# Kernel optimization log

Measured on AMD Instinct MI355X. Metric: run time of the kernel, lower is better.

Reference implementation:

```python
import math
import jax, jax.numpy as jnp
import numpy as np

EMBED = 512
HEADS = 2
HEAD_DIM = EMBED // HEADS


def setup_inputs() -> dict:
    key = jax.random.key(0)
    ks = jax.random.split(key, 10)
    s = 1.0 / math.sqrt(EMBED)
    return {
        "text_embeds": jax.random.normal(ks[0], (64, 32, EMBED), jnp.float32),
        "video_embeds": jax.random.normal(ks[1], (128, 64, EMBED), jnp.float32),
        "Wq": jax.random.normal(ks[2], (EMBED, EMBED), jnp.float32) * s,
        "bq": jnp.zeros((EMBED,), jnp.float32),
        "Wk": jax.random.normal(ks[3], (EMBED, EMBED), jnp.float32) * s,
        "bk": jnp.zeros((EMBED,), jnp.float32),
        "Wv": jax.random.normal(ks[4], (EMBED, EMBED), jnp.float32) * s,
        "bv": jnp.zeros((EMBED,), jnp.float32),
        "Wo": jax.random.normal(ks[5], (EMBED, EMBED), jnp.float32) * s,
        "bo": jnp.zeros((EMBED,), jnp.float32),
    }


def reference(text_embeds, video_embeds, Wq, bq, Wk, bk, Wv, bv, Wo, bo):
    num_texts, num_words, _ = text_embeds.shape
    num_vids, num_frames, _ = video_embeds.shape
    # projections (torch Linear: x @ W.T + b)
    q = (text_embeds @ Wq.T + bq).reshape(num_texts, num_words, HEADS, HEAD_DIM)
    k = (video_embeds @ Wk.T + bk).reshape(num_vids, num_frames, HEADS, HEAD_DIM)
    v = (video_embeds @ Wv.T + bv).reshape(num_vids, num_frames, HEADS, HEAD_DIM)
    # 5D cross attention logits: [vids, texts, heads, frames, words]
    logits = jnp.einsum('avhd,bthd->abhvt', k, q) / math.sqrt(HEAD_DIM)
    weights = jax.nn.softmax(logits, axis=3)  # softmax over frames
    attn = jnp.einsum('avhd,abhvt->abhtd', v, weights)  # [a,b,h,t,d]
    # faithful to torch: reshape (a,b,h,t,d) -> (a,b,t,h*d) in row-major order
    attn = attn.reshape(num_vids, num_texts, num_words, EMBED)
    attn = attn.mean(axis=0)  # [texts, words, embed]
    return attn @ Wo.T + bo
```

## Files before the change

### kernel.cpp

```cpp
#include <hip/hip_runtime.h>
#include <hip/hip_bf16.h>
#include <math.h>

#define EMBED  512
#define HEADS  2
#define HDIM   256
#define NTEXT  64
#define NWORD  32
#define NVID   128
#define NFRM   64

typedef __attribute__((ext_vector_type(8))) short      short8;
typedef __attribute__((ext_vector_type(8))) unsigned short ushort8;
typedef __attribute__((ext_vector_type(4))) float      float4v;
typedef __attribute__((ext_vector_type(4))) unsigned short ushort4v;

__device__ __forceinline__ unsigned short f2bf(float x) {
    __hip_bfloat16 h = __float2bfloat16(x);
    return *(unsigned short*)&h;
}
__device__ __forceinline__ float bf2f(unsigned short u) {
    __hip_bfloat16 h = *(__hip_bfloat16*)&u;
    return __bfloat162float(h);
}

__device__ __forceinline__ void gload_lds16(unsigned short* dst, const unsigned short* src) {
#if __has_builtin(__builtin_amdgcn_global_load_lds)
    __builtin_amdgcn_global_load_lds((const __attribute__((address_space(1))) void*)src,
                                     (__attribute__((address_space(3))) void*)dst,
                                     16, 0, 0);
#else
    *(ushort8*)dst = *(const ushort8*)src;
#endif
}

__global__ __launch_bounds__(256)
void cvt5(const float* __restrict__ s0, const float* __restrict__ s1,
          const float* __restrict__ s2, const float* __restrict__ s3,
          const float* __restrict__ s4, unsigned short* __restrict__ dst) {
    const int y = blockIdx.y;
    const float* s; size_t off; int n4;
    if (y == 0)      { s = s0; off = 0;       n4 = 262144;  }
    else if (y == 1) { s = s1; off = 1048576; n4 = 1048576; }
    else if (y == 2) { s = s2; off = 5242880; n4 = 65536;   }
    else if (y == 3) { s = s3; off = 5505024; n4 = 65536;   }
    else             { s = s4; off = 5767168; n4 = 65536;   }
    unsigned short* d = dst + off;
    for (int i = blockIdx.x * 256 + threadIdx.x; i < n4; i += 512 * 256) {
        float4v f = ((const float4v*)s)[i];
        ((ushort4v*)d)[i] = (ushort4v){f2bf(f.x), f2bf(f.y), f2bf(f.z), f2bf(f.w)};
    }
}

__global__ __launch_bounds__(256)
void proj_qkv(const unsigned short* __restrict__ text, const unsigned short* __restrict__ video,
              const unsigned short* __restrict__ Wqb, const float* __restrict__ bq,
              const unsigned short* __restrict__ Wkb, const float* __restrict__ bk,
              const unsigned short* __restrict__ Wvb, const float* __restrict__ bv,
              unsigned short* __restrict__ qout,
              unsigned short* __restrict__ Kgf, unsigned short* __restrict__ Vgf) {
    const int mb = blockIdx.x, nb = blockIdx.y;
    const int bj = nb * 64;
    const unsigned short *A, *W;
    const float* bias;
    int op, arow, a = 0;
    if (mb < 32)       { op = 0; A = text;  W = Wqb; bias = bq; arow = mb * 64; }
    else if (mb < 160) { op = 1; A = video; W = Wkb; bias = bk; a = mb - 32;  arow = a * 64; }
    else               { op = 2; A = video; W = Wvb; bias = bv; a = mb - 160; arow = a * 64; }

    __shared__ __align__(16) unsigned char smem[32768];
    unsigned short (*Eb)[72] = (unsigned short (*)[72])smem;

    const int tid = threadIdx.x;
    const int w = tid >> 6, lane = tid & 63;
    const int lm = lane & 15, qd = lane >> 4;

    float4v acc[4];
    #pragma unroll
    for (int nt = 0; nt < 4; ++nt) acc[nt] = (float4v){0.f, 0.f, 0.f, 0.f};

    auto STAGE = [&](int buf, int k0) {
        unsigned short* AbL = (unsigned short*)(smem + buf * 16384);
        unsigned short* WbL = (unsigned short*)(smem + buf * 16384 + 8192);
        #pragma unroll
        for (int it = 0; it < 2; ++it) {
            const int s = tid + it * 256;
            const int r = s >> 3, c8 = s & 7;
            const int sc = (c8 ^ (r & 7)) * 8;
            gload_lds16(&AbL[(size_t)s * 8], &A[(size_t)(arow + r) * 512 + k0 + sc]);
            gload_lds16(&WbL[(size_t)s * 8], &W[(size_t)(bj   + r) * 512 + k0 + sc]);
        }
    };

    STAGE(0, 0);
    __syncthreads();
    int cur = 0;
    for (int ks = 0; ks < 8; ++ks) {
        if (ks < 7) STAGE(cur ^ 1, (ks + 1) * 64);
        const unsigned short* AbL = (const unsigned short*)(smem + cur * 16384);
        const unsigned short* WbL = (const unsigned short*)(smem + cur * 16384 + 8192);
        #pragma unroll
        for (int kq = 0; kq < 2; ++kq) {
            const int scol = (kq * 32 + qd * 8) ^ ((lm & 7) * 8);
            const short8 af = *(const short8*)&AbL[(w * 16 + lm) * 64 + scol];
            #pragma unroll
            for (int nt = 0; nt < 4; ++nt) {
                const short8 bf = *(const short8*)&WbL[(nt * 16 + lm) * 64 + scol];
                acc[nt] = __builtin_amdgcn_mfma_f32_16x16x32_bf16(af, bf, acc[nt], 0, 0, 0);
            }
        }
        __syncthreads();
        cur ^= 1;
    }

    if (op == 0) {
        #pragma unroll
        for (int nt = 0; nt < 4; ++nt) {
            const int c = bj + nt * 16 + lm;
            const float bb = bias[c];
            #pragma unroll
            for (int reg = 0; reg < 4; ++reg) {
                const int r = arow + w * 16 + qd * 4 + reg;
                qout[(size_t)r * 512 + c] = f2bf((acc[nt][reg] + bb) * 0.0625f);
            }
        }
        return;
    }

    const int h = bj >> 8;
    const int bj_rel = bj & 255;

    if (op == 1) {
        #pragma unroll
        for (int nt = 0; nt < 4; ++nt) {
            const int dl = nt * 16 + lm;
            const float bb = bias[bj + dl];
            #pragma unroll
            for (int reg = 0; reg < 4; ++reg)
                Eb[w * 16 + qd * 4 + reg][dl] = f2bf(acc[nt][reg] + bb);
        }
        __syncthreads();
        const size_t base = ((size_t)(h * 128 + a)) * 16384;
        #pragma unroll
        for (int i = 0; i < 2; ++i) {
            const int s = tid + i * 256;
            const int ntf = s >> 7, kqr = (s >> 6) & 1, l = s & 63;
            const int v = ntf * 16 + (l & 15);
            const int dl = kqr * 32 + (l >> 4) * 8;
            ushort8 val = *(const ushort8*)&Eb[v][dl];
            *(ushort8*)&Kgf[base + ((size_t)(ntf * 8 + (bj_rel >> 5) + kqr) * 64 + l) * 8] = val;
        }
    } else {
        #pragma unroll
        for (int nt = 0; nt < 4; ++nt) {
            const int dl = nt * 16 + lm;
            const float bb = bias[bj + dl];
            #pragma unroll
            for (int reg = 0; reg < 4; ++reg)
                Eb[dl][w * 16 + qd * 4 + reg] = f2bf(acc[nt][reg] + bb);
        }
        __syncthreads();
        const size_t base = ((size_t)(h * 128 + a)) * 16384;
        #pragma unroll
        for (int i = 0; i < 2; ++i) {
            const int s = tid + i * 256;
            const int ntr = s >> 7, kqv = (s >> 6) & 1, l = s & 63;
            const int dl = ntr * 16 + (l & 15);
            const int v0 = kqv * 32 + (l >> 4) * 8;
            ushort8 val = *(const ushort8*)&Eb[dl][v0];
            *(ushort8*)&Vgf[base + ((size_t)(((bj_rel >> 4) + ntr) * 2 + kqv) * 64 + l) * 8] = val;
        }
    }
}

__global__ __launch_bounds__(512, 2)
void attn9(const unsigned short* __restrict__ Kgf,
           const unsigned short* __restrict__ Vgf,
           const unsigned short* __restrict__ q,
           unsigned short* __restrict__ partg) {
    const int c  = blockIdx.x;
    const int h  = blockIdx.y;
    const int tg = blockIdx.z;
    const int tid = threadIdx.x;
    const int w = tid >> 6, lane = tid & 63;
    const int lm = lane & 15, qd = lane >> 4;
    const int wt = w >> 1;
    const int fh = w & 1;
    const int b = tg * 4 + wt;

    __shared__ __align__(16) unsigned short Kb[2][16384];
    __shared__ __align__(16) unsigned short Vb[2][16384];
    __shared__ __align__(16) unsigned short Pf[4][2][2][512];
    __shared__ __align__(16) float Ex[4][2][2][16][2];

    short8 qf[2][8];
    #pragma unroll
    for (int mt = 0; mt < 2; ++mt)
        #pragma unroll
        for (int kq = 0; kq < 8; ++kq)
            qf[mt][kq] = *(const short8*)
                &q[((size_t)(b * 32 + mt * 16 + lm)) * 512 + h * 256 + kq * 32 + qd * 8];

    float4v pacc[2][8];
    #pragma unroll
    for (int mt = 0; mt < 2; ++mt)
        #pragma unroll
        for (int nd = 0; nd < 8; ++nd) pacc[mt][nd] = (float4v){0.f, 0.f, 0.f, 0.f};

    const size_t vb0 = (size_t)(h * 128 + c * 16) * 16384;

    #pragma unroll
    for (int i = 0; i < 4; ++i) {
        const int s = tid + i * 512;
        gload_lds16(&Kb[0][(size_t)s * 8], &Kgf[vb0 + (size_t)s * 8]);
        gload_lds16(&Vb[0][(size_t)s * 8], &Vgf[vb0 + (size_t)s * 8]);
    }
    #pragma unroll
    for (int i = 0; i < 4; ++i) {
        const int s = tid + i * 512;
        gload_lds16(&Kb[1][(size_t)s * 8], &Kgf[vb0 + 16384 + (size_t)s * 8]);
        gload_lds16(&Vb[1][(size_t)s * 8], &Vgf[vb0 + 16384 + (size_t)s * 8]);
    }
    __syncthreads();

    for (int ai = 0; ai < 16; ++ai) {
        const int cur = ai & 1;

        float4v lacc[2][2];
        #pragma unroll
        for (int nt = 0; nt < 2; ++nt)
            #pragma unroll
            for (int mt = 0; mt < 2; ++mt) lacc[nt][mt] = (float4v){0.f, 0.f, 0.f, 0.f};
        #pragma unroll
        for (int kq = 0; kq < 8; ++kq) {
            #pragma unroll
            for (int nt = 0; nt < 2; ++nt) {
                const short8 kf = *(const short8*)
                    &Kb[cur][(((fh * 2 + nt) * 8 + kq) * 64 + lane) * 8];
                lacc[nt][0] = __builtin_amdgcn_mfma_f32_16x16x32_bf16(kf, qf[0][kq], lacc[nt][0], 0, 0, 0);
                lacc[nt][1] = __builtin_amdgcn_mfma_f32_16x16x32_bf16(kf, qf[1][kq], lacc[nt][1], 0, 0, 0);
            }
        }

        float m2[2], sv[2], e[2][2][4];
        #pragma unroll
        for (int mt = 0; mt < 2; ++mt) {
            float mm = lacc[0][mt][0];
            #pragma unroll
            for (int nt = 0; nt < 2; ++nt)
                #pragma unroll
                for (int r = 0; r < 4; ++r) mm = fmaxf(mm, lacc[nt][mt][r]);
            mm = fmaxf(mm, __shfl_xor(mm, 16));
            mm = fmaxf(mm, __shfl_xor(mm, 32));
            float ss = 0.f;
            #pragma unroll
            for (int nt = 0; nt < 2; ++nt)
                #pragma unroll
                for (int r = 0; r < 4; ++r) {
                    const float ev = __expf(lacc[nt][mt][r] - mm);
                    e[mt][nt][r] = ev;
                    ss += ev;
                }
            ss += __shfl_xor(ss, 16);
            ss += __shfl_xor(ss, 32);
            m2[mt] = mm; sv[mt] = ss;
            if (qd == 0) {
                Ex[wt][fh][mt][lm][0] = mm;
                Ex[wt][fh][mt][lm][1] = ss;
            }
        }
        __syncthreads();

        #pragma unroll
        for (int mt = 0; mt < 2; ++mt) {
            const float om = Ex[wt][fh ^ 1][mt][lm][0];
            const float os = Ex[wt][fh ^ 1][mt][lm][1];
            const float M   = fmaxf(m2[mt], om);
            const float den = sv[mt] * __expf(m2[mt] - M) + os * __expf(om - M);
            const float fac = __expf(m2[mt] - M) / den;
            #pragma unroll
            for (int nt = 0; nt < 2; ++nt) {
                ushort4v pv;
                pv.x = f2bf(e[mt][nt][0] * fac);
                pv.y = f2bf(e[mt][nt][1] * fac);
                pv.z = f2bf(e[mt][nt][2] * fac);
                pv.w = f2bf(e[mt][nt][3] * fac);
                *(ushort4v*)&Pf[wt][mt][fh][(lm + 16 * (nt * 2 + (qd >> 1))) * 8 + (qd & 1) * 4] = pv;
            }
        }
        __syncthreads();

        #pragma unroll
        for (int kqv = 0; kqv < 2; ++kqv) {
            const short8 pf0 = *(const short8*)&Pf[wt][0][kqv][lane * 8];
            const short8 pf1 = *(const short8*)&Pf[wt][1][kqv][lane * 8];
            #pragma unroll
            for (int nd = 0; nd < 8; ++nd) {
                const short8 vf = *(const short8*)
                    &Vb[cur][(((fh * 8 + nd) * 2 + kqv) * 64 + lane) * 8];
                pacc[0][nd] = __builtin_amdgcn_mfma_f32_16x16x32_bf16(pf0, vf, pacc[0][nd], 0, 0, 0);
                pacc[1][nd] = __builtin_amdgcn_mfma_f32_16x16x32_bf16(pf1, vf, pacc[1][nd], 0, 0, 0);
            }
        }
        __syncthreads();

        if (ai < 14) {
            const size_t kb = vb0 + (size_t)(ai + 2) * 16384;
            #pragma unroll
            for (int i = 0; i < 4; ++i) {
                const int s = tid + i * 512;
                gload_lds16(&Kb[cur][(size_t)s * 8], &Kgf[kb + (size_t)s * 8]);
                gload_lds16(&Vb[cur][(size_t)s * 8], &Vgf[kb + (size_t)s * 8]);
            }
        }
    }

    unsigned short* part = partg + (size_t)c * 1048576;
    #pragma unroll
    for (int mt = 0; mt < 2; ++mt)
        #pragma unroll
        for (int nd = 0; nd < 8; ++nd)
            #pragma unroll
            for (int r = 0; r < 4; ++r) {
                const int t = mt * 16 + qd * 4 + r;
                const int d = fh * 128 + nd * 16 + lm;
                const int row = b * 32 + h * 16 + (t >> 1);
                const int col = (t & 1) * 256 + d;
                part[(size_t)row * 512 + col] = f2bf(pacc[mt][nd][r]);
            }
}

__global__ __launch_bounds__(256)
void reduce8(unsigned short* __restrict__ partg) {
    const size_t i = ((size_t)blockIdx.x * 256 + threadIdx.x) * 8;
    float s[8];
    #pragma unroll
    for (int j = 0; j < 8; ++j) s[j] = 0.f;
    #pragma unroll
    for (int p = 0; p < 8; ++p) {
        ushort8 u = *(const ushort8*)&partg[(size_t)p * 1048576 + i];
        #pragma unroll
        for (int j = 0; j < 8; ++j) s[j] += bf2f(u[j]);
    }
    ushort8 o;
    #pragma unroll
    for (int j = 0; j < 8; ++j) o[j] = f2bf(s[j] * 0.0078125f);
    *(ushort8*)&partg[i] = o;
}

__global__ __launch_bounds__(256)
void proj_o(const unsigned short* __restrict__ Abf, const float* __restrict__ W,
            const float* __restrict__ bias, float* __restrict__ C) {
    __shared__ __align__(16) unsigned short Ab[64][72];
    __shared__ __align__(16) unsigned short Wb[64][72];
    const int tid = threadIdx.x;
    const int bi = blockIdx.x * 64, bj = blockIdx.y * 64;
    const int w = tid >> 6, lane = tid & 63;
    const int lm = lane & 15, qd = lane >> 4;

    float4v acc[4];
    #pragma unroll
    for (int nt = 0; nt < 4; ++nt) acc[nt] = (float4v){0.f, 0.f, 0.f, 0.f};

    for (int k0 = 0; k0 < 512; k0 += 64) {
        #pragma unroll
        for (int it = 0; it < 2; ++it) {
            const int s = tid + it * 256;
            const int r = s >> 3, c8 = (s & 7) * 8;
            *(ushort8*)&Ab[r][c8] = *(const ushort8*)&Abf[(size_t)(bi + r) * 512 + k0 + c8];
        }
        #pragma unroll
        for (int it = 0; it < 4; ++it) {
            const int s = tid + it * 256;
            const int r = s >> 4, c4 = (s & 15) * 4;
            float4v fw = *(const float4v*)&W[(size_t)(bj + r) * 512 + k0 + c4];
            *(ushort4v*)&Wb[r][c4] = (ushort4v){f2bf(fw.x), f2bf(fw.y), f2bf(fw.z), f2bf(fw.w)};
        }
        __syncthreads();
        #pragma unroll
        for (int kq = 0; kq < 2; ++kq) {
            const short8 af = *(const short8*)&Ab[w * 16 + lm][kq * 32 + qd * 8];
            #pragma unroll
            for (int nt = 0; nt < 4; ++nt) {
                const short8 bf = *(const short8*)&Wb[nt * 16 + lm][kq * 32 + qd * 8];
                acc[nt] = __builtin_amdgcn_mfma_f32_16x16x32_bf16(af, bf, acc[nt], 0, 0, 0);
            }
        }
        __syncthreads();
    }
    #pragma unroll
    for (int nt = 0; nt < 4; ++nt) {
        const int cc = bj + nt * 16 + lm;
        const float bb = bias[cc];
        #pragma unroll
        for (int reg = 0; reg < 4; ++reg) {
            const int r = bi + w * 16 + qd * 4 + reg;
            C[(size_t)r * 512 + cc] = acc[nt][reg] + bb;
        }
    }
}

extern "C" void kernel_launch(void* const* d_in, const int* in_sizes, int n_in,
                              void* d_out, int out_size, void* d_ws, size_t ws_size,
                              hipStream_t stream) {
    const float* text  = (const float*)d_in[0];
    const float* video = (const float*)d_in[1];
    const float* Wq = (const float*)d_in[2];
    const float* bq = (const float*)d_in[3];
    const float* Wk = (const float*)d_in[4];
    const float* bk = (const float*)d_in[5];
    const float* Wv = (const float*)d_in[6];
    const float* bv = (const float*)d_in[7];
    const float* Wo = (const float*)d_in[8];
    const float* bo = (const float*)d_in[9];

    unsigned short* Kgf   = (unsigned short*)d_ws;
    unsigned short* Vgf   = (unsigned short*)((char*)d_ws + (8u << 20));
    unsigned short* partg = (unsigned short*)((char*)d_ws + (16u << 20));
    unsigned short* textbf  = partg;
    unsigned short* videobf = partg + 1048576;
    unsigned short* wqbf    = partg + 5242880;
    unsigned short* wkbf    = partg + 5505024;
    unsigned short* wvbf    = partg + 5767168;
    unsigned short* qbf   = (unsigned short*)d_out;
    float*          out   = (float*)d_out;

    cvt5<<<dim3(512, 5), 256, 0, stream>>>(text, video, Wq, Wk, Wv, partg);
    proj_qkv<<<dim3(288, 8), 256, 0, stream>>>(textbf, videobf, wqbf, bq, wkbf, bk,
                                               wvbf, bv, qbf, Kgf, Vgf);
    attn9<<<dim3(8, 2, 16), 512, 0, stream>>>(Kgf, Vgf, qbf, partg);
    reduce8<<<dim3(512), 256, 0, stream>>>(partg);
    proj_o<<<dim3(32, 8), 256, 0, stream>>>(partg, Wo, bo, out);
}
```

Baseline: 166.6 us.

## Enlarge QKV projection tiles to 128x128 with 2x2 warp tiling

```diff
diff --git a/kernel.cpp b/kernel.cpp
--- a/kernel.cpp
+++ b/kernel.cpp
@@ -60,35 +60,37 @@
               unsigned short* __restrict__ qout,
               unsigned short* __restrict__ Kgf, unsigned short* __restrict__ Vgf) {
     const int mb = blockIdx.x, nb = blockIdx.y;
-    const int bj = nb * 64;
+    const int bj = nb * 128;
     const unsigned short *A, *W;
     const float* bias;
-    int op, arow, a = 0;
-    if (mb < 32)       { op = 0; A = text;  W = Wqb; bias = bq; arow = mb * 64; }
-    else if (mb < 160) { op = 1; A = video; W = Wkb; bias = bk; a = mb - 32;  arow = a * 64; }
-    else               { op = 2; A = video; W = Wvb; bias = bv; a = mb - 160; arow = a * 64; }
-
-    __shared__ __align__(16) unsigned char smem[32768];
-    unsigned short (*Eb)[72] = (unsigned short (*)[72])smem;
+    int op, arow0, abase = 0;
+    if (mb < 16)      { op = 0; A = text;  W = Wqb; bias = bq; arow0 = mb * 128; }
+    else if (mb < 80) { op = 1; A = video; W = Wkb; bias = bk; abase = (mb - 16) * 2; arow0 = abase * 64; }
+    else              { op = 2; A = video; W = Wvb; bias = bv; abase = (mb - 80) * 2; arow0 = abase * 64; }
+
+    __shared__ __align__(16) unsigned char smem[65536];
 
     const int tid = threadIdx.x;
     const int w = tid >> 6, lane = tid & 63;
     const int lm = lane & 15, qd = lane >> 4;
-
-    float4v acc[4];
-    #pragma unroll
-    for (int nt = 0; nt < 4; ++nt) acc[nt] = (float4v){0.f, 0.f, 0.f, 0.f};
+    const int wr = w >> 1, wc = w & 1;
+
+    float4v acc[4][4];
+    #pragma unroll
+    for (int rt = 0; rt < 4; ++rt)
+        #pragma unroll
+        for (int ct = 0; ct < 4; ++ct) acc[rt][ct] = (float4v){0.f, 0.f, 0.f, 0.f};
 
     auto STAGE = [&](int buf, int k0) {
-        unsigned short* AbL = (unsigned short*)(smem + buf * 16384);
-        unsigned short* WbL = (unsigned short*)(smem + buf * 16384 + 8192);
-        #pragma unroll
-        for (int it = 0; it < 2; ++it) {
+        unsigned short* AbL = (unsigned short*)(smem + buf * 32768);
+        unsigned short* WbL = (unsigned short*)(smem + buf * 32768 + 16384);
+        #pragma unroll
+        for (int it = 0; it < 4; ++it) {
             const int s = tid + it * 256;
             const int r = s >> 3, c8 = s & 7;
             const int sc = (c8 ^ (r & 7)) * 8;
-            gload_lds16(&AbL[(size_t)s * 8], &A[(size_t)(arow + r) * 512 + k0 + sc]);
-            gload_lds16(&WbL[(size_t)s * 8], &W[(size_t)(bj   + r) * 512 + k0 + sc]);
+            gload_lds16(&AbL[(size_t)s * 8], &A[(size_t)(arow0 + r) * 512 + k0 + sc]);
+            gload_lds16(&WbL[(size_t)s * 8], &W[(size_t)(bj    + r) * 512 + k0 + sc]);
         }
     };
 
@@ -97,17 +99,23 @@
     int cur = 0;
     for (int ks = 0; ks < 8; ++ks) {
         if (ks < 7) STAGE(cur ^ 1, (ks + 1) * 64);
-        const unsigned short* AbL = (const unsigned short*)(smem + cur * 16384);
-        const unsigned short* WbL = (const unsigned short*)(smem + cur * 16384 + 8192);
+        const unsigned short* AbL = (const unsigned short*)(smem + cur * 32768);
+        const unsigned short* WbL = (const unsigned short*)(smem + cur * 32768 + 16384);
         #pragma unroll
         for (int kq = 0; kq < 2; ++kq) {
             const int scol = (kq * 32 + qd * 8) ^ ((lm & 7) * 8);
-            const short8 af = *(const short8*)&AbL[(w * 16 + lm) * 64 + scol];
-            #pragma unroll
-            for (int nt = 0; nt < 4; ++nt) {
-                const short8 bf = *(const short8*)&WbL[(nt * 16 + lm) * 64 + scol];
-                acc[nt] = __builtin_amdgcn_mfma_f32_16x16x32_bf16(af, bf, acc[nt], 0, 0, 0);
-            }
+            short8 af[4], bf[4];
+            #pragma unroll
+            for (int rt = 0; rt < 4; ++rt)
+                af[rt] = *(const short8*)&AbL[(wr * 64 + rt * 16 + lm) * 64 + scol];
+            #pragma unroll
+            for (int ct = 0; ct < 4; ++ct)
+                bf[ct] = *(const short8*)&WbL[(wc * 64 + ct * 16 + lm) * 64 + scol];
+            #pragma unroll
+            for (int rt = 0; rt < 4; ++rt)
+                #pragma unroll
+                for (int ct = 0; ct < 4; ++ct)
+                    acc[rt][ct] = __builtin_amdgcn_mfma_f32_16x16x32_bf16(af[rt], bf[ct], acc[rt][ct], 0, 0, 0);
         }
         __syncthreads();
         cur ^= 1;
@@ -115,35 +123,42 @@
 
     if (op == 0) {
         #pragma unroll
-        for (int nt = 0; nt < 4; ++nt) {
-            const int c = bj + nt * 16 + lm;
-            const float bb = bias[c];
-            #pragma unroll
-            for (int reg = 0; reg < 4; ++reg) {
-                const int r = arow + w * 16 + qd * 4 + reg;
-                qout[(size_t)r * 512 + c] = f2bf((acc[nt][reg] + bb) * 0.0625f);
-            }
-        }
+        for (int rt = 0; rt < 4; ++rt)
+            #pragma unroll
+            for (int ct = 0; ct < 4; ++ct) {
+                const int c = bj + wc * 64 + ct * 16 + lm;
+                const float bb = bias[c];
+                #pragma unroll
+                for (int reg = 0; reg < 4; ++reg) {
+                    const int r = arow0 + wr * 64 + rt * 16 + qd * 4 + reg;
+                    qout[(size_t)r * 512 + c] = f2bf((acc[rt][ct][reg] + bb) * 0.0625f);
+                }
+            }
         return;
     }
 
-    const int h = bj >> 8;
-    const int bj_rel = bj & 255;
+    const int a   = abase + wr;
+    const int bjs = bj + wc * 64;
+    const int h      = bjs >> 8;
+    const int bj_rel = bjs & 255;
+    unsigned short (*Eb)[72] = (unsigned short (*)[72])(smem + w * 9216);
+    const size_t base = ((size_t)(h * 128 + a)) * 16384;
 
     if (op == 1) {
         #pragma unroll
-        for (int nt = 0; nt < 4; ++nt) {
-            const int dl = nt * 16 + lm;
-            const float bb = bias[bj + dl];
-            #pragma unroll
-            for (int reg = 0; reg < 4; ++reg)
-                Eb[w * 16 + qd * 4 + reg][dl] = f2bf(acc[nt][reg] + bb);
-        }
-        __syncthreads();
-        const size_t base = ((size_t)(h * 128 + a)) * 16384;
-        #pragma unroll
-        for (int i = 0; i < 2; ++i) {
-            const int s = tid + i * 256;
+        for (int ct = 0; ct < 4; ++ct) {
+            const int dl = ct * 16 + lm;
+            const float bb = bias[bjs + dl];
+            #pragma unroll
+            for (int rt = 0; rt < 4; ++rt)
+                #pragma unroll
+                for (int reg = 0; reg < 4; ++reg)
+                    Eb[rt * 16 + qd * 4 + reg][dl] = f2bf(acc[rt][ct][reg] + bb);
+        }
+        __syncthreads();
+        #pragma unroll
+        for (int it = 0; it < 8; ++it) {
+            const int s = lane + it * 64;
             const int ntf = s >> 7, kqr = (s >> 6) & 1, l = s & 63;
             const int v = ntf * 16 + (l & 15);
             const int dl = kqr * 32 + (l >> 4) * 8;
@@ -152,18 +167,19 @@
         }
     } else {
         #pragma unroll
-        for (int nt = 0; nt < 4; ++nt) {
-            const int dl = nt * 16 + lm;
-            const float bb = bias[bj + dl];
-            #pragma unroll
-            for (int reg = 0; reg < 4; ++reg)
-                Eb[dl][w * 16 + qd * 4 + reg] = f2bf(acc[nt][reg] + bb);
-        }
-        __syncthreads();
-        const size_t base = ((size_t)(h * 128 + a)) * 16384;
-        #pragma unroll
-        for (int i = 0; i < 2; ++i) {
-            const int s = tid + i * 256;
+        for (int ct = 0; ct < 4; ++ct) {
+            const int dl = ct * 16 + lm;
+            const float bb = bias[bjs + dl];
+            #pragma unroll
+            for (int rt = 0; rt < 4; ++rt)
+                #pragma unroll
+                for (int reg = 0; reg < 4; ++reg)
+                    Eb[dl][rt * 16 + qd * 4 + reg] = f2bf(acc[rt][ct][reg] + bb);
+        }
+        __syncthreads();
+        #pragma unroll
+        for (int it = 0; it < 8; ++it) {
+            const int s = lane + it * 64;
             const int ntr = s >> 7, kqv = (s >> 6) & 1, l = s & 63;
             const int dl = ntr * 16 + (l & 15);
             const int v0 = kqv * 32 + (l >> 4) * 8;
@@ -426,7 +442,7 @@
     float*          out   = (float*)d_out;
 
     cvt5<<<dim3(512, 5), 256, 0, stream>>>(text, video, Wq, Wk, Wv, partg);
-    proj_qkv<<<dim3(288, 8), 256, 0, stream>>>(textbf, videobf, wqbf, bq, wkbf, bk,
+    proj_qkv<<<dim3(144, 4), 256, 0, stream>>>(textbf, videobf, wqbf, bq, wkbf, bk,
                                                wvbf, bv, qbf, Kgf, Vgf);
     attn9<<<dim3(8, 2, 16), 512, 0, stream>>>(Kgf, Vgf, qbf, partg);
     reduce8<<<dim3(512), 256, 0, stream>>>(partg);
```

Measured after the change: 167.1 us. About the same (+0.3%).
